# Kernel tuning notes

Measured on AMD Instinct MI355X. Metric: run time of the kernel, lower is better.

## Reference

```python
import jax, jax.numpy as jnp
import numpy as np

B, C, H, W = 2, 128, 64, 256
G, P, EXP = 8, 4, 2
D = C // G


def _conv1x1(x, w, b):
    # x: (b,c,h,w), w: (o,c), b: (o,)
    return jnp.einsum('bchw,oc->bohw', x, w) + b[None, :, None, None]


def _lin_sample(value, x):
    # value: (b,g,d,h,w); x: (b,g,p,h,w) pixel coords along W -> (b,g,d,p,h,w)
    Bv, Gv, Dv, Hv, Wv = value.shape
    Pv = x.shape[2]
    xc = jnp.clip(x, 0.0, Wv - 1.0)
    x0 = jnp.floor(xc)
    i0 = x0.astype(jnp.int32)
    i1 = jnp.minimum(i0 + 1, Wv - 1)
    t = (xc - x0)[:, :, None]  # (b,g,1,p,h,w)
    shape = (Bv, Gv, Dv, Pv, Hv, Wv)
    v = jnp.broadcast_to(value[:, :, :, None], shape)
    v0 = jnp.take_along_axis(v, jnp.broadcast_to(i0[:, :, None], shape), axis=-1)
    v1 = jnp.take_along_axis(v, jnp.broadcast_to(i1[:, :, None], shape), axis=-1)
    return v0 * (1.0 - t) + v1 * t


def _layernorm_c(x, g, b):
    mu = jnp.mean(x, axis=1, keepdims=True)
    var = jnp.mean((x - mu) ** 2, axis=1, keepdims=True)
    return (x - mu) * jax.lax.rsqrt(var + 1e-5) * g[None, :, None, None] + b[None, :, None, None]


def _forward(ml, mr, fl, fr, nl, nr, gml, gmr, cap, gap,
             wv, bv, wn, bn, woc, boc, wog, bog, wa, ba, wo, bo,
             lw, lb, w1, b1, w2, b2):
    mask = jnp.concatenate([gml, gmr], axis=0)   # (2B,1,H,W)
    q = jnp.concatenate([ml, mr], axis=0)        # (2B,C,H,W)
    ctx = jnp.concatenate([fr, fl], axis=0)      # cross: right feats for left queries
    geo = jnp.concatenate([nr, nl], axis=0)      # (2B,3,H,W)
    B2 = q.shape[0]
    # deformable 1D cross-attention (normal-guided)
    value = _conv1x1(ctx, wv, bv).reshape(B2, G, D, H, W)
    nfeat = _conv1x1(geo, wn, bn).reshape(B2, G, D, H, W)
    off_c = _conv1x1(q, woc, boc).reshape(B2, G, P, H, W)
    off_g = _conv1x1(q, wog, bog).reshape(B2, G, P, H, W)
    attn = jax.nn.softmax(_conv1x1(q, wa, ba).reshape(B2, G, 2 * P, H, W), axis=2)
    ctx_kp = jnp.clip(cap * (W - 1.0) + off_c, 0.0, W - 1.0)
    geo_kp = jnp.clip(gap * (W - 1.0) + off_g, 0.0, W - 1.0)
    s_ctx = _lin_sample(value, ctx_kp)           # (2B,G,D,P,H,W)
    s_geo = _lin_sample(nfeat, geo_kp)
    sampled = jnp.concatenate([s_ctx, s_geo], axis=3)  # (2B,G,D,2P,H,W)
    agg = jnp.einsum('bgdphw,bgphw->bgdhw', sampled, attn).reshape(B2, C, H, W)
    upd = _conv1x1(agg, wo, bo) * mask
    # residual + LayerNorm over channels + 1x1-conv FFN
    x = q + upd
    x = _layernorm_c(x, lw, lb)
    h1 = _conv1x1(x, w1, b1)
    x = x + _conv1x1(h1 * jax.nn.sigmoid(h1), w2, b2)
    return x, ctx_kp, geo_kp


def setup_inputs() -> dict:
    key = jax.random.key(0)
    ks = jax.random.split(key, 20)
    f32 = jnp.float32
    def n(k, shape, s=1.0):
        return jax.random.normal(k, shape, dtype=f32) * s
    return {
        'match_left': n(ks[0], (B, C, H, W)),
        'match_right': n(ks[1], (B, C, H, W)),
        'feat_left': n(ks[2], (B, C, H, W)),
        'feat_right': n(ks[3], (B, C, H, W)),
        'normal_left': n(ks[4], (B, 3, H, W)),
        'normal_right': n(ks[5], (B, 3, H, W)),
        'gate_mask_left': jax.random.uniform(ks[6], (B, 1, H, W), dtype=f32),
        'gate_mask_right': jax.random.uniform(ks[7], (B, 1, H, W), dtype=f32),
        'context_anchor_points': jax.random.uniform(ks[8], (2 * B, G, P, H, W), dtype=f32),
        'geometric_anchor_points': jax.random.uniform(ks[9], (2 * B, G, P, H, W), dtype=f32),
        'w_value': n(ks[10], (C, C), 0.02), 'b_value': jnp.zeros((C,), f32),
        'w_normal': n(ks[11], (C, 3), 0.02), 'b_normal': jnp.zeros((C,), f32),
        'w_off_ctx': n(ks[12], (G * P, C), 0.02), 'b_off_ctx': jnp.zeros((G * P,), f32),
        'w_off_geo': n(ks[13], (G * P, C), 0.02), 'b_off_geo': jnp.zeros((G * P,), f32),
        'w_attn': n(ks[14], (G * 2 * P, C), 0.02), 'b_attn': jnp.zeros((G * 2 * P,), f32),
        'w_out': n(ks[15], (C, C), 0.02), 'b_out': jnp.zeros((C,), f32),
        'ln_w': jnp.ones((C,), f32), 'ln_b': jnp.zeros((C,), f32),
        'w_ff1': n(ks[16], (EXP * C, C), 0.02), 'b_ff1': jnp.zeros((EXP * C,), f32),
        'w_ff2': n(ks[17], (C, EXP * C), 0.02), 'b_ff2': jnp.zeros((C,), f32),
    }


def reference(match_left, match_right, feat_left, feat_right, normal_left, normal_right,
              gate_mask_left, gate_mask_right, context_anchor_points, geometric_anchor_points,
              w_value, b_value, w_normal, b_normal, w_off_ctx, b_off_ctx, w_off_geo, b_off_geo,
              w_attn, b_attn, w_out, b_out, ln_w, ln_b, w_ff1, b_ff1, w_ff2, b_ff2):
    x, ckp, gkp = _forward(match_left, match_right, feat_left, feat_right, normal_left, normal_right,
                           gate_mask_left, gate_mask_right, context_anchor_points, geometric_anchor_points,
                           w_value, b_value, w_normal, b_normal, w_off_ctx, b_off_ctx, w_off_geo, b_off_geo,
                           w_attn, b_attn, w_out, b_out, ln_w, ln_b, w_ff1, b_ff1, w_ff2, b_ff2)
    ml, mr = jnp.split(x, 2, axis=0)
    return (ml, mr, ckp, gkp)
```

## Files before the change

### kernel.cpp

```cpp
#include <hip/hip_runtime.h>
#include <cstdint>
#include <math.h>

#define B2v 4
#define Cc  128
#define Hh  64
#define Ww  256
#define Gg  8
#define Pp  4
#define HW  (Hh*Ww)
#define CHW (Cc*HW)
#define PIT 136

typedef float f32x4 __attribute__((ext_vector_type(4)));
typedef short s16x8 __attribute__((ext_vector_type(8)));
typedef short s16x4 __attribute__((ext_vector_type(4)));

__device__ __forceinline__ short f2bf(float x) {
    union { float f; unsigned u; } a; a.f = x;
    unsigned r = a.u + 0x7fffu + ((a.u >> 16) & 1u);
    return (short)(r >> 16);
}
__device__ __forceinline__ float bf2f(short s) {
    union { unsigned u; float f; } a; a.u = ((unsigned)(unsigned short)s) << 16;
    return a.f;
}
__device__ __forceinline__ unsigned pack2_bf(float f0, float f1) {
    union { float f; unsigned u; } a, b; a.f = f0; b.f = f1;
    return __builtin_amdgcn_perm(b.u, a.u, 0x07060302);
}

__global__ __launch_bounds__(256) void prep_kernel(
    const float* __restrict__ wv, const float* __restrict__ woc,
    const float* __restrict__ wog, const float* __restrict__ wa,
    const float* __restrict__ wo, const float* __restrict__ w1,
    const float* __restrict__ w2,
    const float* __restrict__ boc, const float* __restrict__ bog,
    const float* __restrict__ ba,
    short* __restrict__ wbf, float* __restrict__ bq)
{
    int i = blockIdx.x * 256 + threadIdx.x;
    if (i < 16384) wbf[i] = f2bf(wv[i]);
    else if (i < 32768) {
        int j = i - 16384; int r = j >> 7, c = j & 127;
        float v = (r < 32) ? woc[r * 128 + c] : (r < 64) ? wog[(r - 32) * 128 + c]
                                              : wa[(r - 64) * 128 + c];
        wbf[i] = f2bf(v);
    }
    else if (i < 49152)  wbf[i] = f2bf(wo[i - 32768]);
    else if (i < 81920)  wbf[i] = f2bf(w1[i - 49152]);
    else if (i < 114688) wbf[i] = f2bf(w2[i - 81920]);
    else if (i < 114816) {
        int r = i - 114688;
        bq[r] = (r < 32) ? boc[r] : (r < 64) ? bog[r - 32] : ba[r - 64];
    }
}

__global__ __launch_bounds__(512, 2) void mega_kernel(
    const float* __restrict__ mlq, const float* __restrict__ mrq,
    const float* __restrict__ fl,  const float* __restrict__ fr,
    const float* __restrict__ nl,  const float* __restrict__ nr,
    const float* __restrict__ gml, const float* __restrict__ gmr,
    const float* __restrict__ cap, const float* __restrict__ gap,
    const short* __restrict__ wbf, const float* __restrict__ bq,
    const float* __restrict__ bv,
    const float* __restrict__ wn,  const float* __restrict__ bn,
    const float* __restrict__ bo,
    const float* __restrict__ lnw, const float* __restrict__ lnb,
    const float* __restrict__ b1,  const float* __restrict__ b2,
    float* __restrict__ out_ml, float* __restrict__ out_mr,
    float* __restrict__ ckp_out, float* __restrict__ gkp_out)
{
    __shared__ short buf1[256 * PIT];
    __shared__ short buf2[256 * PIT];
    __shared__ float sgeo[3 * 256];
    __shared__ float swn4[128 * 4];
    __shared__ float redS[512], redQ[512];
    __shared__ float smu[256], srs[256];

    const short* wv_bf = wbf;
    const short* wq_bf = wbf + 16384;
    const short* wo_bf = wbf + 32768;
    const short* w1_bf = wbf + 49152;
    const short* w2_bf = wbf + 81920;

    const int t    = threadIdx.x;
    const int lane = t & 63;
    const int ww   = t >> 6;
    const int lm   = lane & 15;
    const int lq   = lane >> 4;
    const int h = blockIdx.x, b = blockIdx.y;
    const int hWw = h * Ww;
    const int px   = t & 255;
    const int half = t >> 8;

    const float* ctx = (b < 2) ? fr + (size_t)b * CHW : fl + (size_t)(b - 2) * CHW;
    const float* q   = (b < 2) ? mlq + (size_t)b * CHW : mrq + (size_t)(b - 2) * CHW;
    const float* geo = (b < 2) ? nr + (size_t)b * 3 * HW : nl + (size_t)(b - 2) * 3 * HW;
    const float* msk = (b < 2) ? gml + (size_t)b * HW : gmr + (size_t)(b - 2) * HW;
    float* outp = (b < 2) ? out_ml + (size_t)b * CHW : out_mr + (size_t)(b - 2) * CHW;

    for (int i = t; i < 768; i += 512) sgeo[i] = geo[(size_t)(i >> 8) * HW + hWw + (i & 255)];
    if (t < 128) {
        swn4[t * 4 + 0] = wn[t * 3 + 0];
        swn4[t * 4 + 1] = wn[t * 3 + 1];
        swn4[t * 4 + 2] = wn[t * 3 + 2];
        swn4[t * 4 + 3] = bn[t];
    }

    {
        const int c0 = ww * 16;
#pragma unroll
        for (int sub = 0; sub < 4; sub++) {
            const int p = sub * 64 + lane;
            const size_t base = (size_t)c0 * HW + hWw + p;
#pragma unroll
            for (int k = 0; k < 8; k++) {
                float f0 = ctx[base + (size_t)(2 * k) * HW];
                float f1 = ctx[base + (size_t)(2 * k + 1) * HW];
                *(unsigned*)(&buf1[p * PIT + c0 + 2 * k]) = pack2_bf(f0, f1);
            }
        }
    }
    __syncthreads();

    {
        f32x4 acc[16];
#pragma unroll
        for (int nt = 0; nt < 16; nt++) acc[nt] = (f32x4){0.f, 0.f, 0.f, 0.f};
#pragma unroll
        for (int kk = 0; kk < 4; kk++) {
            s16x8 a = *(const s16x8*)(wv_bf + (size_t)(ww * 16 + lm) * 128 + kk * 32 + lq * 8);
#pragma unroll
            for (int nt = 0; nt < 16; nt++) {
                s16x8 bfv = *(const s16x8*)(&buf1[(nt * 16 + lm) * PIT + kk * 32 + lq * 8]);
                acc[nt] = __builtin_amdgcn_mfma_f32_16x16x32_bf16(a, bfv, acc[nt], 0, 0, 0);
            }
        }
        const int ob = ww * 16 + lq * 4;
        float bias[4];
#pragma unroll
        for (int r = 0; r < 4; r++) bias[r] = bv[ob + r];
#pragma unroll
        for (int nt = 0; nt < 16; nt++) {
            const int wg = nt * 16 + lm;
            s16x4 pk;
#pragma unroll
            for (int r = 0; r < 4; r++) pk[r] = f2bf(acc[nt][r] + bias[r]);
            *(s16x4*)(&buf2[wg * PIT + ob]) = pk;
        }
    }
    __syncthreads();

    {
        const int c0 = ww * 16;
#pragma unroll
        for (int sub = 0; sub < 4; sub++) {
            const int p = sub * 64 + lane;
            const size_t base = (size_t)c0 * HW + hWw + p;
#pragma unroll
            for (int k = 0; k < 8; k++) {
                float f0 = q[base + (size_t)(2 * k) * HW];
                float f1 = q[base + (size_t)(2 * k + 1) * HW];
                *(unsigned*)(&buf1[p * PIT + c0 + 2 * k]) = pack2_bf(f0, f1);
            }
        }
    }
    __syncthreads();

    {
        f32x4 acc[16];
#pragma unroll
        for (int nt = 0; nt < 16; nt++) acc[nt] = (f32x4){0.f, 0.f, 0.f, 0.f};
#pragma unroll
        for (int kk = 0; kk < 4; kk++) {
            s16x8 a = *(const s16x8*)(wq_bf + (size_t)(ww * 16 + lm) * 128 + kk * 32 + lq * 8);
#pragma unroll
            for (int nt = 0; nt < 16; nt++) {
                s16x8 bfv = *(const s16x8*)(&buf1[(nt * 16 + lm) * PIT + kk * 32 + lq * 8]);
                acc[nt] = __builtin_amdgcn_mfma_f32_16x16x32_bf16(a, bfv, acc[nt], 0, 0, 0);
            }
        }
        __syncthreads();
        const int ob = ww * 16 + lq * 4;
        float bias[4];
#pragma unroll
        for (int r = 0; r < 4; r++) bias[r] = bq[ob + r];
#pragma unroll
        for (int nt = 0; nt < 16; nt++) {
            const int wg = nt * 16 + lm;
            s16x4 pk;
#pragma unroll
            for (int r = 0; r < 4; r++) pk[r] = f2bf(acc[nt][r] + bias[r]);
            *(s16x4*)(&buf1[wg * PIT + ob]) = pk;
        }
    }
    __syncthreads();

    float attnr[4][8], kpr[4][8];
#pragma unroll
    for (int gi = 0; gi < 4; gi++) {
        const int g = half * 4 + gi;
        s16x8 lg = *(const s16x8*)(&buf1[px * PIT + 64 + g * 8]);
        float L[8], m = -1e30f;
#pragma unroll
        for (int j = 0; j < 8; j++) { L[j] = bf2f(lg[j]); m = fmaxf(m, L[j]); }
        float s = 0.f;
#pragma unroll
        for (int j = 0; j < 8; j++) { L[j] = expf(L[j] - m); s += L[j]; }
        float inv = 1.f / s;
#pragma unroll
        for (int j = 0; j < 8; j++) attnr[gi][j] = L[j] * inv;
#pragma unroll
        for (int p = 0; p < 4; p++) {
            size_t kidx = ((((size_t)b * Gg + g) * Pp + p) * Hh + h) * Ww + px;
            float oc = bf2f(buf1[px * PIT + g * 4 + p]);
            float og = bf2f(buf1[px * PIT + 32 + g * 4 + p]);
            float ck = fminf(fmaxf(cap[kidx] * 255.0f + oc, 0.f), 255.f);
            float gk = fminf(fmaxf(gap[kidx] * 255.0f + og, 0.f), 255.f);
            ckp_out[kidx] = ck;
            gkp_out[kidx] = gk;
            kpr[gi][p] = ck;
            kpr[gi][4 + p] = gk;
        }
    }
    __syncthreads();

#pragma unroll
    for (int gi = 0; gi < 4; gi++) {
        const int g = half * 4 + gi;
        float a16[16];
#pragma unroll
        for (int d = 0; d < 16; d++) a16[d] = 0.f;
#pragma unroll
        for (int j = 0; j < 4; j++) {
            float x = kpr[gi][j];
            int i0 = (int)floorf(x);
            int i1 = min(i0 + 1, Ww - 1);
            float tt = x - (float)i0;
            float c0 = attnr[gi][j] * (1.f - tt);
            float c1 = attnr[gi][j] * tt;
            s16x8 v0a = *(const s16x8*)(&buf2[i0 * PIT + g * 16]);
            s16x8 v0b = *(const s16x8*)(&buf2[i0 * PIT + g * 16 + 8]);
            s16x8 v1a = *(const s16x8*)(&buf2[i1 * PIT + g * 16]);
            s16x8 v1b = *(const s16x8*)(&buf2[i1 * PIT + g * 16 + 8]);
#pragma unroll
            for (int d = 0; d < 8; d++) {
                a16[d]     += c0 * bf2f(v0a[d]) + c1 * bf2f(v1a[d]);
                a16[8 + d] += c0 * bf2f(v0b[d]) + c1 * bf2f(v1b[d]);
            }
        }
        {
            float gs0 = 0.f, gs1 = 0.f, gs2 = 0.f, as = 0.f;
#pragma unroll
            for (int j = 4; j < 8; j++) {
                float x = kpr[gi][j];
                int i0 = (int)floorf(x);
                int i1 = min(i0 + 1, Ww - 1);
                float tt = x - (float)i0;
                float c0 = attnr[gi][j] * (1.f - tt);
                float c1 = attnr[gi][j] * tt;
                gs0 += c0 * sgeo[i0] + c1 * sgeo[i1];
                gs1 += c0 * sgeo[256 + i0] + c1 * sgeo[256 + i1];
                gs2 += c0 * sgeo[512 + i0] + c1 * sgeo[512 + i1];
                as  += attnr[gi][j];
            }
#pragma unroll
            for (int d = 0; d < 16; d++) {
                const float* w4 = &swn4[(g * 16 + d) * 4];
                a16[d] += w4[0] * gs0 + w4[1] * gs1 + w4[2] * gs2 + w4[3] * as;
            }
        }
        s16x8 p0, p1;
#pragma unroll
        for (int d = 0; d < 8; d++) { p0[d] = f2bf(a16[d]); p1[d] = f2bf(a16[8 + d]); }
        *(s16x8*)(&buf1[px * PIT + g * 16])     = p0;
        *(s16x8*)(&buf1[px * PIT + g * 16 + 8]) = p1;
    }
    __syncthreads();

    {
        f32x4 acc1[16];
#pragma unroll
        for (int nt = 0; nt < 16; nt++) acc1[nt] = (f32x4){0.f, 0.f, 0.f, 0.f};
#pragma unroll
        for (int kk = 0; kk < 4; kk++) {
            s16x8 a = *(const s16x8*)(wo_bf + (size_t)(ww * 16 + lm) * 128 + kk * 32 + lq * 8);
#pragma unroll
            for (int nt = 0; nt < 16; nt++) {
                s16x8 bfv = *(const s16x8*)(&buf1[(nt * 16 + lm) * PIT + kk * 32 + lq * 8]);
                acc1[nt] = __builtin_amdgcn_mfma_f32_16x16x32_bf16(a, bfv, acc1[nt], 0, 0, 0);
            }
        }
        __syncthreads();
        const int ob = ww * 16 + lq * 4;
        float bias[4];
#pragma unroll
        for (int r = 0; r < 4; r++) bias[r] = bo[ob + r];
#pragma unroll
        for (int nt = 0; nt < 16; nt++) {
            const int wg = nt * 16 + lm;
            float mval = msk[hWw + wg];
            s16x4 pk;
#pragma unroll
            for (int r = 0; r < 4; r++) {
                float upd = acc1[nt][r] + bias[r];
                float qv = q[(size_t)(ob + r) * HW + hWw + wg];
                pk[r] = f2bf(qv + upd * mval);
            }
            *(s16x4*)(&buf1[wg * PIT + ob]) = pk;
        }
    }
    __syncthreads();

    {
        float ls = 0.f, lsq = 0.f;
#pragma unroll
        for (int c8 = 0; c8 < 8; c8++) {
            s16x8 v = *(const s16x8*)(&buf1[px * PIT + half * 64 + c8 * 8]);
#pragma unroll
            for (int j = 0; j < 8; j++) { float f = bf2f(v[j]); ls += f; lsq += f * f; }
        }
        redS[t] = ls; redQ[t] = lsq;
        __syncthreads();
        if (t < 256) {
            float s  = redS[t] + redS[t + 256];
            float qq = redQ[t] + redQ[t + 256];
            float mu = s * (1.f / 128.f);
            float var = qq * (1.f / 128.f) - mu * mu;
            smu[t] = mu;
            srs[t] = rsqrtf(var + 1e-5f);
        }
        __syncthreads();
        const float mu = smu[px], rs = srs[px];
#pragma unroll
        for (int c8 = 0; c8 < 8; c8++) {
            s16x8 v = *(const s16x8*)(&buf1[px * PIT + half * 64 + c8 * 8]);
            s16x8 pk;
#pragma unroll
            for (int j = 0; j < 8; j++) {
                int c = half * 64 + c8 * 8 + j;
                pk[j] = f2bf((bf2f(v[j]) - mu) * rs * lnw[c] + lnb[c]);
            }
            *(s16x8*)(&buf1[px * PIT + half * 64 + c8 * 8]) = pk;
        }
    }
    __syncthreads();

    f32x4 acc3[16];
#pragma unroll
    for (int nt = 0; nt < 16; nt++) acc3[nt] = (f32x4){0.f, 0.f, 0.f, 0.f};

    for (int jc = 0; jc < 2; jc++) {
        f32x4 acc2[16];
#pragma unroll
        for (int nt = 0; nt < 16; nt++) acc2[nt] = (f32x4){0.f, 0.f, 0.f, 0.f};
#pragma unroll
        for (int kk = 0; kk < 4; kk++) {
            s16x8 a = *(const s16x8*)(w1_bf + (size_t)(jc * 128 + ww * 16 + lm) * 128 + kk * 32 + lq * 8);
#pragma unroll
            for (int nt = 0; nt < 16; nt++) {
                s16x8 bfv = *(const s16x8*)(&buf1[(nt * 16 + lm) * PIT + kk * 32 + lq * 8]);
                acc2[nt] = __builtin_amdgcn_mfma_f32_16x16x32_bf16(a, bfv, acc2[nt], 0, 0, 0);
            }
        }
        {
            const int jb = ww * 16 + lq * 4;
            float bias[4];
#pragma unroll
            for (int r = 0; r < 4; r++) bias[r] = b1[jc * 128 + jb + r];
#pragma unroll
            for (int nt = 0; nt < 16; nt++) {
                const int wg = nt * 16 + lm;
                s16x4 pk;
#pragma unroll
                for (int r = 0; r < 4; r++) {
                    float hv = acc2[nt][r] + bias[r];
                    pk[r] = f2bf(hv / (1.f + expf(-hv)));
                }
                *(s16x4*)(&buf2[wg * PIT + jb]) = pk;
            }
        }
        __syncthreads();
#pragma unroll
        for (int kk = 0; kk < 4; kk++) {
            s16x8 a = *(const s16x8*)(w2_bf + (size_t)(ww * 16 + lm) * 256 + jc * 128 + kk * 32 + lq * 8);
#pragma unroll
            for (int nt = 0; nt < 16; nt++) {
                s16x8 bfv = *(const s16x8*)(&buf2[(nt * 16 + lm) * PIT + kk * 32 + lq * 8]);
                acc3[nt] = __builtin_amdgcn_mfma_f32_16x16x32_bf16(a, bfv, acc3[nt], 0, 0, 0);
            }
        }
        __syncthreads();
    }

    {
        const int ob = ww * 16 + lq * 4;
        float b2v[4];
#pragma unroll
        for (int r = 0; r < 4; r++) b2v[r] = b2[ob + r];
#pragma unroll
        for (int nt = 0; nt < 16; nt++) {
            const int wg = nt * 16 + lm;
            s16x4 xn4 = *(const s16x4*)(&buf1[wg * PIT + ob]);
#pragma unroll
            for (int r = 0; r < 4; r++)
                outp[(size_t)(ob + r) * HW + hWw + wg] = bf2f(xn4[r]) + b2v[r] + acc3[nt][r];
        }
    }
}

extern "C" void kernel_launch(void* const* d_in, const int* in_sizes, int n_in,
                              void* d_out, int out_size, void* d_ws, size_t ws_size,
                              hipStream_t stream)
{
    const float* match_l = (const float*)d_in[0];
    const float* match_r = (const float*)d_in[1];
    const float* feat_l  = (const float*)d_in[2];
    const float* feat_r  = (const float*)d_in[3];
    const float* norm_l  = (const float*)d_in[4];
    const float* norm_r  = (const float*)d_in[5];
    const float* gml     = (const float*)d_in[6];
    const float* gmr     = (const float*)d_in[7];
    const float* cap     = (const float*)d_in[8];
    const float* gap     = (const float*)d_in[9];
    const float* wv  = (const float*)d_in[10]; const float* bv  = (const float*)d_in[11];
    const float* wn  = (const float*)d_in[12]; const float* bn  = (const float*)d_in[13];
    const float* woc = (const float*)d_in[14]; const float* boc = (const float*)d_in[15];
    const float* wog = (const float*)d_in[16]; const float* bog = (const float*)d_in[17];
    const float* wa  = (const float*)d_in[18]; const float* ba  = (const float*)d_in[19];
    const float* wo  = (const float*)d_in[20]; const float* bo  = (const float*)d_in[21];
    const float* lnw = (const float*)d_in[22]; const float* lnb = (const float*)d_in[23];
    const float* w1  = (const float*)d_in[24]; const float* b1  = (const float*)d_in[25];
    const float* w2  = (const float*)d_in[26]; const float* b2  = (const float*)d_in[27];

    float* out = (float*)d_out;
    float* out_ml  = out;
    float* out_mr  = out + (size_t)2 * CHW;
    float* ckp_out = out + (size_t)4 * CHW;
    float* gkp_out = ckp_out + (size_t)B2v * Gg * Pp * HW;

    float* ws = (float*)d_ws;
    float* bq  = ws;
    short* wbf = (short*)(bq + 128);

    prep_kernel<<<dim3(449), dim3(256), 0, stream>>>(
        wv, woc, wog, wa, wo, w1, w2, boc, bog, ba, wbf, bq);
    mega_kernel<<<dim3(Hh, B2v), dim3(512), 0, stream>>>(
        match_l, match_r, feat_l, feat_r, norm_l, norm_r, gml, gmr, cap, gap,
        wbf, bq, bv, wn, bn, bo, lnw, lnb, b1, b2,
        out_ml, out_mr, ckp_out, gkp_out);
}
```

Measured before the change: 222.3 us.

## Merge value and query projections into one staged GEMM pass, vectorize bf16 unpacking

Loads the context and query tiles together into two LDS buffers and runs the value and query 1x1-conv MFMA loops in one pass. This drops one load phase and two barriers and swaps the roles of buf1 and buf2 in later stages. It also prefetches the anchor points into registers early, uses __expf for softmax and SiLU, removes one barrier after the output projection, and replaces per-element bf16 conversions with packed 32-bit unpack/pack helpers. The fused GEMM doubles the live accumulator registers, which may lower occupancy or cause spills.

```diff
diff --git a/kernel.cpp b/kernel.cpp
--- a/kernel.cpp
+++ b/kernel.cpp
@@ -13,8 +13,11 @@
 #define PIT 136
 
 typedef float f32x4 __attribute__((ext_vector_type(4)));
+typedef float f32x2 __attribute__((ext_vector_type(2)));
 typedef short s16x8 __attribute__((ext_vector_type(8)));
 typedef short s16x4 __attribute__((ext_vector_type(4)));
+typedef unsigned u32x2 __attribute__((ext_vector_type(2)));
+typedef unsigned u32x4 __attribute__((ext_vector_type(4)));
 
 __device__ __forceinline__ short f2bf(float x) {
     union { float f; unsigned u; } a; a.f = x;
@@ -28,6 +31,11 @@
 __device__ __forceinline__ unsigned pack2_bf(float f0, float f1) {
     union { float f; unsigned u; } a, b; a.f = f0; b.f = f1;
     return __builtin_amdgcn_perm(b.u, a.u, 0x07060302);
+}
+__device__ __forceinline__ f32x2 bf2_lohi(unsigned d) {
+    union { unsigned u; float f; } lo, hi;
+    lo.u = d << 16; hi.u = d & 0xffff0000u;
+    return (f32x2){lo.f, hi.f};
 }
 
 __global__ __launch_bounds__(256) void prep_kernel(
@@ -100,6 +108,18 @@
     const float* msk = (b < 2) ? gml + (size_t)b * HW : gmr + (size_t)(b - 2) * HW;
     float* outp = (b < 2) ? out_ml + (size_t)b * CHW : out_mr + (size_t)(b - 2) * CHW;
 
+    float capr[16], gapr[16];
+#pragma unroll
+    for (int gi = 0; gi < 4; gi++) {
+        const int g = half * 4 + gi;
+#pragma unroll
+        for (int p = 0; p < 4; p++) {
+            size_t kidx = ((((size_t)b * Gg + g) * Pp + p) * Hh + h) * Ww + px;
+            capr[gi * 4 + p] = cap[kidx];
+            gapr[gi * 4 + p] = gap[kidx];
+        }
+    }
+
     for (int i = t; i < 768; i += 512) sgeo[i] = geo[(size_t)(i >> 8) * HW + hWw + (i & 255)];
     if (t < 128) {
         swn4[t * 4 + 0] = wn[t * 3 + 0];
@@ -116,83 +136,52 @@
             const size_t base = (size_t)c0 * HW + hWw + p;
 #pragma unroll
             for (int k = 0; k < 8; k++) {
-                float f0 = ctx[base + (size_t)(2 * k) * HW];
-                float f1 = ctx[base + (size_t)(2 * k + 1) * HW];
-                *(unsigned*)(&buf1[p * PIT + c0 + 2 * k]) = pack2_bf(f0, f1);
-            }
+                float c0f = ctx[base + (size_t)(2 * k) * HW];
+                float c1f = ctx[base + (size_t)(2 * k + 1) * HW];
+                float q0f = q[base + (size_t)(2 * k) * HW];
+                float q1f = q[base + (size_t)(2 * k + 1) * HW];
+                *(unsigned*)(&buf1[p * PIT + c0 + 2 * k]) = pack2_bf(c0f, c1f);
+                *(unsigned*)(&buf2[p * PIT + c0 + 2 * k]) = pack2_bf(q0f, q1f);
+            }
+        }
+    }
+    __syncthreads();
+
+    f32x4 accV[16], accP[16];
+#pragma unroll
+    for (int nt = 0; nt < 16; nt++) {
+        accV[nt] = (f32x4){0.f, 0.f, 0.f, 0.f};
+        accP[nt] = (f32x4){0.f, 0.f, 0.f, 0.f};
+    }
+#pragma unroll
+    for (int kk = 0; kk < 4; kk++) {
+        s16x8 aV = *(const s16x8*)(wv_bf + (size_t)(ww * 16 + lm) * 128 + kk * 32 + lq * 8);
+        s16x8 aP = *(const s16x8*)(wq_bf + (size_t)(ww * 16 + lm) * 128 + kk * 32 + lq * 8);
+#pragma unroll
+        for (int nt = 0; nt < 16; nt++) {
+            s16x8 bV = *(const s16x8*)(&buf1[(nt * 16 + lm) * PIT + kk * 32 + lq * 8]);
+            s16x8 bP = *(const s16x8*)(&buf2[(nt * 16 + lm) * PIT + kk * 32 + lq * 8]);
+            accV[nt] = __builtin_amdgcn_mfma_f32_16x16x32_bf16(aV, bV, accV[nt], 0, 0, 0);
+            accP[nt] = __builtin_amdgcn_mfma_f32_16x16x32_bf16(aP, bP, accP[nt], 0, 0, 0);
         }
     }
     __syncthreads();
 
     {
-        f32x4 acc[16];
-#pragma unroll
-        for (int nt = 0; nt < 16; nt++) acc[nt] = (f32x4){0.f, 0.f, 0.f, 0.f};
-#pragma unroll
-        for (int kk = 0; kk < 4; kk++) {
-            s16x8 a = *(const s16x8*)(wv_bf + (size_t)(ww * 16 + lm) * 128 + kk * 32 + lq * 8);
-#pragma unroll
-            for (int nt = 0; nt < 16; nt++) {
-                s16x8 bfv = *(const s16x8*)(&buf1[(nt * 16 + lm) * PIT + kk * 32 + lq * 8]);
-                acc[nt] = __builtin_amdgcn_mfma_f32_16x16x32_bf16(a, bfv, acc[nt], 0, 0, 0);
-            }
-        }
         const int ob = ww * 16 + lq * 4;
-        float bias[4];
-#pragma unroll
-        for (int r = 0; r < 4; r++) bias[r] = bv[ob + r];
+        float bvv[4], bqv[4];
+#pragma unroll
+        for (int r = 0; r < 4; r++) { bvv[r] = bv[ob + r]; bqv[r] = bq[ob + r]; }
 #pragma unroll
         for (int nt = 0; nt < 16; nt++) {
             const int wg = nt * 16 + lm;
-            s16x4 pk;
-#pragma unroll
-            for (int r = 0; r < 4; r++) pk[r] = f2bf(acc[nt][r] + bias[r]);
-            *(s16x4*)(&buf2[wg * PIT + ob]) = pk;
-        }
-    }
-    __syncthreads();
-
-    {
-        const int c0 = ww * 16;
-#pragma unroll
-        for (int sub = 0; sub < 4; sub++) {
-            const int p = sub * 64 + lane;
-            const size_t base = (size_t)c0 * HW + hWw + p;
-#pragma unroll
-            for (int k = 0; k < 8; k++) {
-                float f0 = q[base + (size_t)(2 * k) * HW];
-                float f1 = q[base + (size_t)(2 * k + 1) * HW];
-                *(unsigned*)(&buf1[p * PIT + c0 + 2 * k]) = pack2_bf(f0, f1);
-            }
-        }
-    }
-    __syncthreads();
-
-    {
-        f32x4 acc[16];
-#pragma unroll
-        for (int nt = 0; nt < 16; nt++) acc[nt] = (f32x4){0.f, 0.f, 0.f, 0.f};
-#pragma unroll
-        for (int kk = 0; kk < 4; kk++) {
-            s16x8 a = *(const s16x8*)(wq_bf + (size_t)(ww * 16 + lm) * 128 + kk * 32 + lq * 8);
-#pragma unroll
-            for (int nt = 0; nt < 16; nt++) {
-                s16x8 bfv = *(const s16x8*)(&buf1[(nt * 16 + lm) * PIT + kk * 32 + lq * 8]);
-                acc[nt] = __builtin_amdgcn_mfma_f32_16x16x32_bf16(a, bfv, acc[nt], 0, 0, 0);
-            }
-        }
-        __syncthreads();
-        const int ob = ww * 16 + lq * 4;
-        float bias[4];
-#pragma unroll
-        for (int r = 0; r < 4; r++) bias[r] = bq[ob + r];
-#pragma unroll
-        for (int nt = 0; nt < 16; nt++) {
-            const int wg = nt * 16 + lm;
-            s16x4 pk;
-#pragma unroll
-            for (int r = 0; r < 4; r++) pk[r] = f2bf(acc[nt][r] + bias[r]);
-            *(s16x4*)(&buf1[wg * PIT + ob]) = pk;
+            u32x2 pv, pp;
+            pv[0] = pack2_bf(accV[nt][0] + bvv[0], accV[nt][1] + bvv[1]);
+            pv[1] = pack2_bf(accV[nt][2] + bvv[2], accV[nt][3] + bvv[3]);
+            pp[0] = pack2_bf(accP[nt][0] + bqv[0], accP[nt][1] + bqv[1]);
+            pp[1] = pack2_bf(accP[nt][2] + bqv[2], accP[nt][3] + bqv[3]);
+            *(u32x2*)(&buf1[wg * PIT + ob]) = pv;
+            *(u32x2*)(&buf2[wg * PIT + ob]) = pp;
         }
     }
     __syncthreads();
@@ -201,23 +190,23 @@
 #pragma unroll
     for (int gi = 0; gi < 4; gi++) {
         const int g = half * 4 + gi;
-        s16x8 lg = *(const s16x8*)(&buf1[px * PIT + 64 + g * 8]);
+        s16x8 lg = *(const s16x8*)(&buf2[px * PIT + 64 + g * 8]);
         float L[8], m = -1e30f;
 #pragma unroll
         for (int j = 0; j < 8; j++) { L[j] = bf2f(lg[j]); m = fmaxf(m, L[j]); }
         float s = 0.f;
 #pragma unroll
-        for (int j = 0; j < 8; j++) { L[j] = expf(L[j] - m); s += L[j]; }
+        for (int j = 0; j < 8; j++) { L[j] = __expf(L[j] - m); s += L[j]; }
         float inv = 1.f / s;
 #pragma unroll
         for (int j = 0; j < 8; j++) attnr[gi][j] = L[j] * inv;
 #pragma unroll
         for (int p = 0; p < 4; p++) {
             size_t kidx = ((((size_t)b * Gg + g) * Pp + p) * Hh + h) * Ww + px;
-            float oc = bf2f(buf1[px * PIT + g * 4 + p]);
-            float og = bf2f(buf1[px * PIT + 32 + g * 4 + p]);
-            float ck = fminf(fmaxf(cap[kidx] * 255.0f + oc, 0.f), 255.f);
-            float gk = fminf(fmaxf(gap[kidx] * 255.0f + og, 0.f), 255.f);
+            float oc = bf2f(buf2[px * PIT + g * 4 + p]);
+            float og = bf2f(buf2[px * PIT + 32 + g * 4 + p]);
+            float ck = fminf(fmaxf(capr[gi * 4 + p] * 255.0f + oc, 0.f), 255.f);
+            float gk = fminf(fmaxf(gapr[gi * 4 + p] * 255.0f + og, 0.f), 255.f);
             ckp_out[kidx] = ck;
             gkp_out[kidx] = gk;
             kpr[gi][p] = ck;
@@ -229,25 +218,26 @@
 #pragma unroll
     for (int gi = 0; gi < 4; gi++) {
         const int g = half * 4 + gi;
-        float a16[16];
-#pragma unroll
-        for (int d = 0; d < 16; d++) a16[d] = 0.f;
+        f32x2 a2[8];
+#pragma unroll
+        for (int k = 0; k < 8; k++) a2[k] = (f32x2){0.f, 0.f};
 #pragma unroll
         for (int j = 0; j < 4; j++) {
             float x = kpr[gi][j];
             int i0 = (int)floorf(x);
             int i1 = min(i0 + 1, Ww - 1);
             float tt = x - (float)i0;
-            float c0 = attnr[gi][j] * (1.f - tt);
-            float c1 = attnr[gi][j] * tt;
-            s16x8 v0a = *(const s16x8*)(&buf2[i0 * PIT + g * 16]);
-            s16x8 v0b = *(const s16x8*)(&buf2[i0 * PIT + g * 16 + 8]);
-            s16x8 v1a = *(const s16x8*)(&buf2[i1 * PIT + g * 16]);
-            s16x8 v1b = *(const s16x8*)(&buf2[i1 * PIT + g * 16 + 8]);
-#pragma unroll
-            for (int d = 0; d < 8; d++) {
-                a16[d]     += c0 * bf2f(v0a[d]) + c1 * bf2f(v1a[d]);
-                a16[8 + d] += c0 * bf2f(v0b[d]) + c1 * bf2f(v1b[d]);
+            float w0 = attnr[gi][j] * (1.f - tt);
+            float w1v = attnr[gi][j] * tt;
+            f32x2 c0 = (f32x2){w0, w0}, c1 = (f32x2){w1v, w1v};
+            const u32x4* p0 = (const u32x4*)(&buf1[i0 * PIT + g * 16]);
+            const u32x4* p1 = (const u32x4*)(&buf1[i1 * PIT + g * 16]);
+            u32x4 d0a = p0[0], d0b = p0[1];
+            u32x4 d1a = p1[0], d1b = p1[1];
+#pragma unroll
+            for (int k = 0; k < 4; k++) {
+                a2[k]     += c0 * bf2_lohi(d0a[k]) + c1 * bf2_lohi(d1a[k]);
+                a2[4 + k] += c0 * bf2_lohi(d0b[k]) + c1 * bf2_lohi(d1b[k]);
             }
         }
         {
@@ -266,16 +256,21 @@
                 as  += attnr[gi][j];
             }
 #pragma unroll
-            for (int d = 0; d < 16; d++) {
-                const float* w4 = &swn4[(g * 16 + d) * 4];
-                a16[d] += w4[0] * gs0 + w4[1] * gs1 + w4[2] * gs2 + w4[3] * as;
-            }
-        }
-        s16x8 p0, p1;
-#pragma unroll
-        for (int d = 0; d < 8; d++) { p0[d] = f2bf(a16[d]); p1[d] = f2bf(a16[8 + d]); }
-        *(s16x8*)(&buf1[px * PIT + g * 16])     = p0;
-        *(s16x8*)(&buf1[px * PIT + g * 16 + 8]) = p1;
+            for (int k = 0; k < 8; k++) {
+                const float* wa4 = &swn4[(g * 16 + 2 * k) * 4];
+                const float* wb4 = wa4 + 4;
+                a2[k].x += wa4[0] * gs0 + wa4[1] * gs1 + wa4[2] * gs2 + wa4[3] * as;
+                a2[k].y += wb4[0] * gs0 + wb4[1] * gs1 + wb4[2] * gs2 + wb4[3] * as;
+            }
+        }
+        u32x4 pk0;
+#pragma unroll
+        for (int k = 0; k < 4; k++) pk0[k] = pack2_bf(a2[k].x, a2[k].y);
+        u32x4 pk1;
+#pragma unroll
+        for (int k = 0; k < 4; k++) pk1[k] = pack2_bf(a2[4 + k].x, a2[4 + k].y);
+        *(u32x4*)(&buf2[px * PIT + g * 16])     = pk0;
+        *(u32x4*)(&buf2[px * PIT + g * 16 + 8]) = pk1;
     }
     __syncthreads();
 
@@ -288,11 +283,10 @@
             s16x8 a = *(const s16x8*)(wo_bf + (size_t)(ww * 16 + lm) * 128 + kk * 32 + lq * 8);
 #pragma unroll
             for (int nt = 0; nt < 16; nt++) {
-                s16x8 bfv = *(const s16x8*)(&buf1[(nt * 16 + lm) * PIT + kk * 32 + lq * 8]);
+                s16x8 bfv = *(const s16x8*)(&buf2[(nt * 16 + lm) * PIT + kk * 32 + lq * 8]);
                 acc1[nt] = __builtin_amdgcn_mfma_f32_16x16x32_bf16(a, bfv, acc1[nt], 0, 0, 0);
             }
         }
-        __syncthreads();
         const int ob = ww * 16 + lq * 4;
         float bias[4];
 #pragma unroll
@@ -301,14 +295,14 @@
         for (int nt = 0; nt < 16; nt++) {
             const int wg = nt * 16 + lm;
             float mval = msk[hWw + wg];
-            s16x4 pk;
-#pragma unroll
-            for (int r = 0; r < 4; r++) {
-                float upd = acc1[nt][r] + bias[r];
-                float qv = q[(size_t)(ob + r) * HW + hWw + wg];
-                pk[r] = f2bf(qv + upd * mval);
-            }
-            *(s16x4*)(&buf1[wg * PIT + ob]) = pk;
+            float x0 = q[(size_t)(ob + 0) * HW + hWw + wg] + (acc1[nt][0] + bias[0]) * mval;
+            float x1 = q[(size_t)(ob + 1) * HW + hWw + wg] + (acc1[nt][1] + bias[1]) * mval;
+            float x2 = q[(size_t)(ob + 2) * HW + hWw + wg] + (acc1[nt][2] + bias[2]) * mval;
+            float x3 = q[(size_t)(ob + 3) * HW + hWw + wg] + (acc1[nt][3] + bias[3]) * mval;
+            u32x2 pk;
+            pk[0] = pack2_bf(x0, x1);
+            pk[1] = pack2_bf(x2, x3);
+            *(u32x2*)(&buf1[wg * PIT + ob]) = pk;
         }
     }
     __syncthreads();
@@ -316,10 +310,12 @@
     {
         float ls = 0.f, lsq = 0.f;
 #pragma unroll
-        for (int c8 = 0; c8 < 8; c8++) {
-            s16x8 v = *(const s16x8*)(&buf1[px * PIT + half * 64 + c8 * 8]);
-#pragma unroll
-            for (int j = 0; j < 8; j++) { float f = bf2f(v[j]); ls += f; lsq += f * f; }
+        for (int c4 = 0; c4 < 16; c4++) {
+            unsigned d = *(const unsigned*)(&buf1[px * PIT + half * 64 + c4 * 4]);
+            unsigned d2 = *(const unsigned*)(&buf1[px * PIT + half * 64 + c4 * 4 + 2]);
+            f32x2 v = bf2_lohi(d), v2 = bf2_lohi(d2);
+            ls += v.x + v.y + v2.x + v2.y;
+            lsq += v.x * v.x + v.y * v.y + v2.x * v2.x + v2.y * v2.y;
         }
         redS[t] = ls; redQ[t] = lsq;
         __syncthreads();
@@ -335,14 +331,17 @@
         const float mu = smu[px], rs = srs[px];
 #pragma unroll
         for (int c8 = 0; c8 < 8; c8++) {
-            s16x8 v = *(const s16x8*)(&buf1[px * PIT + half * 64 + c8 * 8]);
-            s16x8 pk;
-#pragma unroll
-            for (int j = 0; j < 8; j++) {
-                int c = half * 64 + c8 * 8 + j;
-                pk[j] = f2bf((bf2f(v[j]) - mu) * rs * lnw[c] + lnb[c]);
-            }
-            *(s16x8*)(&buf1[px * PIT + half * 64 + c8 * 8]) = pk;
+            const int c = half * 64 + c8 * 8;
+            u32x4 d = *(const u32x4*)(&buf1[px * PIT + c]);
+            u32x4 o;
+#pragma unroll
+            for (int k = 0; k < 4; k++) {
+                f32x2 v = bf2_lohi(d[k]);
+                float y0 = (v.x - mu) * rs * lnw[c + 2 * k] + lnb[c + 2 * k];
+                float y1 = (v.y - mu) * rs * lnw[c + 2 * k + 1] + lnb[c + 2 * k + 1];
+                o[k] = pack2_bf(y0, y1);
+            }
+            *(u32x4*)(&buf1[px * PIT + c]) = o;
         }
     }
     __syncthreads();
@@ -372,13 +371,16 @@
 #pragma unroll
             for (int nt = 0; nt < 16; nt++) {
                 const int wg = nt * 16 + lm;
-                s16x4 pk;
+                float hv[4];
 #pragma unroll
                 for (int r = 0; r < 4; r++) {
-                    float hv = acc2[nt][r] + bias[r];
-                    pk[r] = f2bf(hv / (1.f + expf(-hv)));
+                    float x = acc2[nt][r] + bias[r];
+                    hv[r] = x / (1.f + __expf(-x));
                 }
-                *(s16x4*)(&buf2[wg * PIT + jb]) = pk;
+                u32x2 pk;
+                pk[0] = pack2_bf(hv[0], hv[1]);
+                pk[1] = pack2_bf(hv[2], hv[3]);
+                *(u32x2*)(&buf2[wg * PIT + jb]) = pk;
             }
         }
         __syncthreads();
@@ -402,10 +404,12 @@
 #pragma unroll
         for (int nt = 0; nt < 16; nt++) {
             const int wg = nt * 16 + lm;
-            s16x4 xn4 = *(const s16x4*)(&buf1[wg * PIT + ob]);
-#pragma unroll
-            for (int r = 0; r < 4; r++)
-                outp[(size_t)(ob + r) * HW + hWw + wg] = bf2f(xn4[r]) + b2v[r] + acc3[nt][r];
+            u32x2 d = *(const u32x2*)(&buf1[wg * PIT + ob]);
+            f32x2 xa = bf2_lohi(d[0]), xb = bf2_lohi(d[1]);
+            outp[(size_t)(ob + 0) * HW + hWw + wg] = xa.x + b2v[0] + acc3[nt][0];
+            outp[(size_t)(ob + 1) * HW + hWw + wg] = xa.y + b2v[1] + acc3[nt][1];
+            outp[(size_t)(ob + 2) * HW + hWw + wg] = xb.x + b2v[2] + acc3[nt][2];
+            outp[(size_t)(ob + 3) * HW + hWw + wg] = xb.y + b2v[3] + acc3[nt][3];
         }
     }
 }
```

Measured after the change: 236.0 us. 1.06x slower.
